# Optimization experiments

Hardware: AMD Instinct MI355X
Metric: run time of the kernel (lower is better)

Reference implementation:

```python
import jax, jax.numpy as jnp
import numpy as np

BS = 2048   # batch, iterated sequentially (memory carried step to step)
M = 256     # memory_size
E = 128     # expanded_memory_emb_size
HS = 512    # summarizer_hidden_size
HA = 512    # shared_AC_hidden_size
HP = 256    # processor_hidden_size


def make_pe(max_len, d):
    # standard sinusoidal positional encoding [max_len, d]
    pos = np.arange(max_len, dtype=np.float32)[:, None]
    div = np.exp(np.arange(0, d, 2, dtype=np.float32) * (-np.log(10000.0) / d))
    pe = np.zeros((max_len, d), dtype=np.float32)
    pe[:, 0::2] = np.sin(pos * div)
    pe[:, 1::2] = np.cos(pos * div)
    return jnp.asarray(pe)


def setup_inputs() -> dict:
    key = jax.random.key(0)
    ks = jax.random.split(key, 32)

    def n(k, sh, s=0.05):
        return jax.random.normal(k, sh, dtype=jnp.float32) * s

    return {
        "state": jax.random.normal(ks[0], (BS, 4), dtype=jnp.float32),
        "memory0": jax.random.uniform(ks[1], (M, E), dtype=jnp.float32),  # buffer init U(0,1)
        # embedder: Linear(4, E)
        "W_emb": n(ks[2], (4, E)), "b_emb": n(ks[3], (E,)),
        # reader Summarizer MLP: E -> HS -> 1
        "Wr1": n(ks[4], (E, HS)), "br1": n(ks[5], (HS,)),
        "Wr2": n(ks[6], (HS, 1)), "br2": n(ks[7], (1,)),
        # writer Summarizer MLP: E -> HS -> M
        "Ww1": n(ks[8], (E, HS)), "bw1": n(ks[9], (HS,)),
        "Ww2": n(ks[10], (HS, M)), "bw2": n(ks[11], (M,)),
        # shared AC trunk: 2E -> HA
        "Ws": n(ks[12], (2 * E, HA)), "bs_": n(ks[13], (HA,)),
        # actor: HA -> 5, critic: HA -> 1
        "Wa": n(ks[14], (HA, 5)), "ba": n(ks[15], (5,)),
        "Wc": n(ks[16], (HA, 1)), "bc": n(ks[17], (1,)),
        # processor: (5 + 1 + 2E) -> HP -> E
        "Wp1": n(ks[18], (5 + 1 + 2 * E, HP)), "bp1": n(ks[19], (HP,)),
        "Wp2": n(ks[20], (HP, E)), "bp2": n(ks[21], (E,)),
    }


def reference(state, memory0, W_emb, b_emb, Wr1, br1, Wr2, br2,
              Ww1, bw1, Ww2, bw2, Ws, bs_, Wa, ba, Wc, bc,
              Wp1, bp1, Wp2, bp2):
    pe_mem = make_pe(M, E)  # PE added to the M memory slots
    sg = jax.lax.stop_gradient

    def summarize(x, W1, b1, W2, b2):
        # Summarizer (MLP method): weight = softmax over token axis, z = weight^T x
        w = jax.nn.softmax(jax.nn.relu(x @ W1 + b1) @ W2 + b2, axis=0)  # [T, K]
        return w.T @ x  # [K, E]

    se = state @ W_emb + b_emb  # embed once: [BS, E]

    def step(mem, s):
        # reader over [current state ; PE(memory)] -> single summary token
        xr = jnp.concatenate([s[None, :], mem + pe_mem], axis=0)        # [M+1, E]
        mem_state = summarize(xr, Wr1, br1, Wr2, br2)[0]                # [E]
        cstate = jnp.concatenate([s, mem_state])                        # concat=True -> [2E]
        h = jax.nn.relu(cstate @ Ws + bs_)                              # [HA]
        probs = jax.nn.softmax(h @ Wa + ba)                             # [5]
        val = h @ Wc + bc                                               # [1]
        pin = jnp.concatenate([s, mem_state, probs, val])               # [2E+6]
        ms2 = jax.nn.relu(pin @ Wp1 + bp1) @ Wp2 + bp2                  # processed mem_state [E]
        # writer sees detached state / mem_state / memory (torch .detach())
        xw = jnp.concatenate([sg(s)[None, :], sg(ms2)[None, :], sg(mem) + pe_mem], axis=0)  # [M+2, E]
        nm = summarize(xw, Ww1, bw1, Ww2, bw2)                          # [M, E]
        nm = nm - nm.min(axis=-1, keepdims=True)
        nm = nm / nm.max(axis=-1, keepdims=True)
        return nm, (probs, val)

    _, (action_probs, state_values) = jax.lax.scan(step, memory0, se)
    return action_probs, state_values  # [BS, 5], [BS, 1]
```

## Files before the change

### kernel.cpp

```cpp
#include <hip/hip_runtime.h>
#include <math.h>

#define BSZ 2048
#define MM  256
#define EE  128
#define HSS 512
#define HPP 256
#define NOWN 64
#define NBLK 129
#define LEADER 128
#define TPB 512
#define ROWS 4

typedef float f4 __attribute__((ext_vector_type(4)));

#define OFF_PE   512
#define OFF_R0   (OFF_PE + MM*EE)
#define OFF_W0   (OFF_R0 + BSZ)
#define OFF_MP   (OFF_W0 + BSZ*MM)
#define OFF_SW   (OFF_MP + 2*MM*EE)
#define OFF_EV   (OFF_SW + 2*MM*MM)
#define OFF_ES   (OFF_EV + NOWN*EE)
#define OFF_MS2  (OFF_ES + NOWN)
#define OFF_CS   (OFF_MS2 + EE)
#define OFF_CBS  (OFF_CS + 4*HSS)
#define OFF_CP   (OFF_CBS + HSS)
#define OFF_CBP  (OFF_CP + 4*HPP)
#define OFF_BD   (OFF_CBP + HPP)
#define OFF_BP   (OFF_BD + NOWN*ROWS)

struct KParams {
  const float *state, *mem0, *Wemb, *bemb, *Wr1, *br1, *Wr2, *br2;
  const float *Ww1, *bw1, *Ww2, *bw2, *Ws, *bs, *Wa, *ba, *Wc, *bc;
  const float *Wp1, *bp1, *Wp2, *bp2;
  float *out;
  float *ws;
};

__device__ __forceinline__ float ldA(const float* p) {
  return __hip_atomic_load(p, __ATOMIC_RELAXED, __HIP_MEMORY_SCOPE_AGENT);
}
__device__ __forceinline__ void stA(float* p, float v) {
  __hip_atomic_store(p, v, __ATOMIC_RELAXED, __HIP_MEMORY_SCOPE_AGENT);
}
__device__ __forceinline__ unsigned ldAu(const unsigned* p) {
  return __hip_atomic_load(p, __ATOMIC_RELAXED, __HIP_MEMORY_SCOPE_AGENT);
}
__device__ __forceinline__ void stAu(unsigned* p, unsigned v) {
  __hip_atomic_store(p, v, __ATOMIC_RELAXED, __HIP_MEMORY_SCOPE_AGENT);
}

__device__ __forceinline__ void ldA4x8(const float* p, int strideF, f4* v) {
  const float *p1=p+strideF, *p2=p+2*strideF, *p3=p+3*strideF,
              *p4=p+4*strideF, *p5=p+5*strideF, *p6=p+6*strideF, *p7=p+7*strideF;
  asm volatile(
    "global_load_dwordx4 %0, %8, off sc0 sc1\n\t"
    "global_load_dwordx4 %1, %9, off sc0 sc1\n\t"
    "global_load_dwordx4 %2, %10, off sc0 sc1\n\t"
    "global_load_dwordx4 %3, %11, off sc0 sc1\n\t"
    "global_load_dwordx4 %4, %12, off sc0 sc1\n\t"
    "global_load_dwordx4 %5, %13, off sc0 sc1\n\t"
    "global_load_dwordx4 %6, %14, off sc0 sc1\n\t"
    "global_load_dwordx4 %7, %15, off sc0 sc1\n\t"
    "s_waitcnt vmcnt(0)"
    : "=&v"(v[0]), "=&v"(v[1]), "=&v"(v[2]), "=&v"(v[3]),
      "=&v"(v[4]), "=&v"(v[5]), "=&v"(v[6]), "=&v"(v[7])
    : "v"(p), "v"(p1), "v"(p2), "v"(p3), "v"(p4), "v"(p5), "v"(p6), "v"(p7)
    : "memory");
}
__device__ __forceinline__ void ldA4x4(const float* p, int strideF, f4* v) {
  const float *p1=p+strideF, *p2=p+2*strideF, *p3=p+3*strideF;
  asm volatile(
    "global_load_dwordx4 %0, %4, off sc0 sc1\n\t"
    "global_load_dwordx4 %1, %5, off sc0 sc1\n\t"
    "global_load_dwordx4 %2, %6, off sc0 sc1\n\t"
    "global_load_dwordx4 %3, %7, off sc0 sc1\n\t"
    "s_waitcnt vmcnt(0)"
    : "=&v"(v[0]), "=&v"(v[1]), "=&v"(v[2]), "=&v"(v[3])
    : "v"(p), "v"(p1), "v"(p2), "v"(p3)
    : "memory");
}
__device__ __forceinline__ f4 ldA4(const float* p) {
  f4 r;
  asm volatile("global_load_dwordx4 %0, %1, off sc0 sc1\n\ts_waitcnt vmcnt(0)"
    : "=&v"(r) : "v"(p) : "memory");
  return r;
}

__device__ __forceinline__ void drainSync() {
  asm volatile("s_waitcnt vmcnt(0)" ::: "memory");
  __syncthreads();
}

__device__ __forceinline__ float brs(float v, float* s8, int tid) {
  for (int o = 32; o > 0; o >>= 1) v += __shfl_down(v, o, 64);
  __syncthreads();
  if ((tid & 63) == 0) s8[tid >> 6] = v;
  __syncthreads();
  float r = s8[0]+s8[1]+s8[2]+s8[3]+s8[4]+s8[5]+s8[6]+s8[7];
  __syncthreads();
  return r;
}

template<int N>
__device__ __forceinline__ void brsN(float* v, float* sred, int tid) {
  #pragma unroll
  for (int k = 0; k < N; ++k)
    for (int o = 32; o > 0; o >>= 1) v[k] += __shfl_down(v[k], o, 64);
  __syncthreads();
  if ((tid & 63) == 0) {
    const int w = tid >> 6;
    #pragma unroll
    for (int k = 0; k < N; ++k) sred[k*8 + w] = v[k];
  }
  __syncthreads();
  #pragma unroll
  for (int k = 0; k < N; ++k) {
    float s = sred[k*8 + 0];
    #pragma unroll
    for (int w = 1; w < 8; ++w) s += sred[k*8 + w];
    v[k] = s;
  }
  __syncthreads();
}

__global__ __launch_bounds__(TPB)
void toyac_kernel(KParams p) {
  const int g = blockIdx.x;
  const int tid = threadIdx.x;
  float* ws = p.ws;
  unsigned* bar = (unsigned*)p.ws;
  const int og = (g >= NOWN && g < LEADER) ? (g - NOWN) : g;
  const int c0 = ROWS * ((g < NOWN) ? g : og);

  __shared__ float sX[ROWS][EE];
  __shared__ float sBuf[8192];
  __shared__ float sH4[ROWS][HSS];
  __shared__ float sHms[HSS];
  __shared__ float sEv[ROWS][MM];
  __shared__ float sRed[16];
  __shared__ float s8[8];
  __shared__ float sR48[48];
  __shared__ float sMS[EE];
  __shared__ float sMS2[EE];
  __shared__ float sSE[EE];
  __shared__ float sP1[HPP];
  __shared__ float sHv[HSS];
  __shared__ float sD[ROWS];
  __shared__ float sSm[32];

  const int hq = (tid & 127) * 4;
  const int eg4 = tid >> 7;

  if (g < NOWN) {
    const int e = tid & 127, r = tid >> 7, c = c0 + r;
    double dv = exp(-(double)(2*(e>>1)) * log(10000.0) / 128.0);
    double arg = (double)c * dv;
    float pev = ((e & 1) == 0) ? (float)sin(arg) : (float)cos(arg);
    ws[OFF_PE + (size_t)c*EE + e] = pev;
    float m0v = p.mem0[(size_t)c*EE + e] + pev;
    stA(ws + OFF_MP + (size_t)c*EE + e, m0v);
    sX[r][e] = m0v;
  } else if (g == LEADER) {
    for (int jj = tid; jj < HSS; jj += TPB) {
      float a0=0.f,a1=0.f,a2=0.f,a3=0.f,cb=0.f;
      for (int e = 0; e < EE; ++e) {
        float wv = p.Ws[(size_t)e*HSS + jj];
        a0 += p.Wemb[e]*wv; a1 += p.Wemb[EE+e]*wv;
        a2 += p.Wemb[2*EE+e]*wv; a3 += p.Wemb[3*EE+e]*wv;
        cb += p.bemb[e]*wv;
      }
      ws[OFF_CS + jj] = a0; ws[OFF_CS + HSS + jj] = a1;
      ws[OFF_CS + 2*HSS + jj] = a2; ws[OFF_CS + 3*HSS + jj] = a3;
      ws[OFF_CBS + jj] = cb;
    }
    if (tid < HPP) {
      int k = tid;
      float a0=0.f,a1=0.f,a2=0.f,a3=0.f,cb=0.f;
      for (int e = 0; e < EE; ++e) {
        float wv = p.Wp1[(size_t)e*HPP + k];
        a0 += p.Wemb[e]*wv; a1 += p.Wemb[EE+e]*wv;
        a2 += p.Wemb[2*EE+e]*wv; a3 += p.Wemb[3*EE+e]*wv;
        cb += p.bemb[e]*wv;
      }
      ws[OFF_CP + k] = a0; ws[OFF_CP + HPP + k] = a1;
      ws[OFF_CP + 2*HPP + k] = a2; ws[OFF_CP + 3*HPP + k] = a3;
      ws[OFF_CBP + k] = cb;
    }
  }

  for (int t = g; t < BSZ; t += NBLK) {
    __syncthreads();
    if (tid < EE) {
      const float* st = p.state + (size_t)t*4;
      sSE[tid] = st[0]*p.Wemb[tid] + st[1]*p.Wemb[EE+tid]
               + st[2]*p.Wemb[2*EE+tid] + st[3]*p.Wemb[3*EE+tid] + p.bemb[tid];
    }
    __syncthreads();
    {
      f4 a = {0.f,0.f,0.f,0.f};
      const float* base = p.Wr1 + (size_t)(eg4*32)*HSS + hq;
      for (int i = 0; i < 32; ++i)
        a += sSE[eg4*32 + i] * (*(const f4*)(base + (size_t)i*HSS));
      *(f4*)(sBuf + (size_t)eg4*HSS + hq) = a;
      __syncthreads();
      int h = tid;
      float hid = sBuf[h] + sBuf[HSS+h] + sBuf[2*HSS+h] + sBuf[3*HSS+h] + p.br1[h];
      float v = fmaxf(hid, 0.f) * p.Wr2[h];
      float sc = brs(v, s8, tid);
      if (tid == 0) stA(ws + OFF_R0 + t, sc + p.br2[0]);
      __syncthreads();
    }
    {
      f4 a = {0.f,0.f,0.f,0.f};
      const float* base = p.Ww1 + (size_t)(eg4*32)*HSS + hq;
      for (int i = 0; i < 32; ++i)
        a += sSE[eg4*32 + i] * (*(const f4*)(base + (size_t)i*HSS));
      *(f4*)(sBuf + (size_t)eg4*HSS + hq) = a;
      __syncthreads();
      int h = tid;
      sHv[h] = fmaxf(sBuf[h] + sBuf[HSS+h] + sBuf[2*HSS+h] + sBuf[3*HSS+h] + p.bw1[h], 0.f);
      __syncthreads();
      const int cq = (tid & 63) * 4, hg = tid >> 6;
      f4 q = {0.f,0.f,0.f,0.f};
      const float* b2 = p.Ww2 + (size_t)(hg*64)*MM + cq;
      for (int i = 0; i < 64; ++i)
        q += sHv[hg*64 + i] * (*(const f4*)(b2 + (size_t)i*MM));
      *(f4*)(sBuf + (size_t)hg*MM + cq) = q;
      __syncthreads();
      if (tid < MM) {
        float s = 0.f;
        #pragma unroll
        for (int k = 0; k < 8; ++k) s += sBuf[(size_t)k*MM + tid];
        stA(ws + OFF_W0 + (size_t)t*MM + tid, s + p.bw2[tid]);
      }
      __syncthreads();
    }
  }

  auto stageA = [&]() {
    {
      f4 a0={0.f,0.f,0.f,0.f},a1=a0,a2=a0,a3=a0;
      const float* base = p.Wr1 + (size_t)(eg4*32)*HSS + hq;
      for (int i = 0; i < 32; ++i) {
        f4 w = *(const f4*)(base + (size_t)i*HSS);
        int e = eg4*32 + i;
        a0 += sX[0][e]*w; a1 += sX[1][e]*w; a2 += sX[2][e]*w; a3 += sX[3][e]*w;
      }
      *(f4*)(sBuf + ((size_t)eg4*ROWS + 0)*HSS + hq) = a0;
      *(f4*)(sBuf + ((size_t)eg4*ROWS + 1)*HSS + hq) = a1;
      *(f4*)(sBuf + ((size_t)eg4*ROWS + 2)*HSS + hq) = a2;
      *(f4*)(sBuf + ((size_t)eg4*ROWS + 3)*HSS + hq) = a3;
    }
    __syncthreads();
    float es[ROWS];
    {
      int h = tid;
      float b = p.br1[h], wr = p.Wr2[h];
      float sc[ROWS];
      #pragma unroll
      for (int r = 0; r < ROWS; ++r) {
        float hid = sBuf[(0*ROWS+r)*HSS+h] + sBuf[(1*ROWS+r)*HSS+h]
                  + sBuf[(2*ROWS+r)*HSS+h] + sBuf[(3*ROWS+r)*HSS+h] + b;
        sc[r] = fmaxf(hid, 0.f) * wr;
      }
      brsN<ROWS>(sc, sR48, tid);
      #pragma unroll
      for (int r = 0; r < ROWS; ++r) es[r] = expf(sc[r] + p.br2[0]);
    }
    if (tid < EE) {
      float v = es[0]*sX[0][tid] + es[1]*sX[1][tid] + es[2]*sX[2][tid] + es[3]*sX[3][tid];
      stA(ws + OFF_EV + (size_t)g*EE + tid, v);
    }
    if (tid == 0) stA(ws + OFF_ES + g, es[0]+es[1]+es[2]+es[3]);
  };

  auto stageC = [&](float* swdst) {
    {
      f4 a0={0.f,0.f,0.f,0.f},a1=a0,a2=a0,a3=a0;
      const float* base = p.Ww1 + (size_t)(eg4*32)*HSS + hq;
      for (int i = 0; i < 32; ++i) {
        f4 w = *(const f4*)(base + (size_t)i*HSS);
        int e = eg4*32 + i;
        a0 += sX[0][e]*w; a1 += sX[1][e]*w; a2 += sX[2][e]*w; a3 += sX[3][e]*w;
      }
      *(f4*)(sBuf + ((size_t)eg4*ROWS + 0)*HSS + hq) = a0;
      *(f4*)(sBuf + ((size_t)eg4*ROWS + 1)*HSS + hq) = a1;
      *(f4*)(sBuf + ((size_t)eg4*ROWS + 2)*HSS + hq) = a2;
      *(f4*)(sBuf + ((size_t)eg4*ROWS + 3)*HSS + hq) = a3;
    }
    __syncthreads();
    {
      int h = tid;
      float b = p.bw1[h];
      #pragma unroll
      for (int r = 0; r < ROWS; ++r)
        sH4[r][h] = fmaxf(sBuf[(0*ROWS+r)*HSS+h] + sBuf[(1*ROWS+r)*HSS+h]
                        + sBuf[(2*ROWS+r)*HSS+h] + sBuf[(3*ROWS+r)*HSS+h] + b, 0.f);
    }
    __syncthreads();
    {
      const int cq = (tid & 63) * 4, hg = tid >> 6;
      f4 q0={0.f,0.f,0.f,0.f},q1=q0,q2=q0,q3=q0;
      const float* b2 = p.Ww2 + (size_t)(hg*64)*MM + cq;
      for (int i = 0; i < 64; ++i) {
        f4 w = *(const f4*)(b2 + (size_t)i*MM);
        int h = hg*64 + i;
        q0 += sH4[0][h]*w; q1 += sH4[1][h]*w; q2 += sH4[2][h]*w; q3 += sH4[3][h]*w;
      }
      *(f4*)(sBuf + ((size_t)hg*ROWS + 0)*MM + cq) = q0;
      *(f4*)(sBuf + ((size_t)hg*ROWS + 1)*MM + cq) = q1;
      *(f4*)(sBuf + ((size_t)hg*ROWS + 2)*MM + cq) = q2;
      *(f4*)(sBuf + ((size_t)hg*ROWS + 3)*MM + cq) = q3;
    }
    __syncthreads();
    {
      const int col = tid & 255, rp = tid >> 8;
      #pragma unroll
      for (int rr = 0; rr < 2; ++rr) {
        int r = rp*2 + rr;
        float s = 0.f;
        #pragma unroll
        for (int k = 0; k < 8; ++k) s += sBuf[((size_t)k*ROWS + r)*MM + col];
        stA(swdst + (size_t)(c0 + r)*MM + col, s + p.bw2[col]);
      }
    }
  };

  auto dBulkH = [&](int t) {
    float* swc = ws + OFF_SW + (size_t)(t&1)*MM*MM;
    float* mpc = ws + OFF_MP + (size_t)(t&1)*MM*EE;
    float ex[ROWS] = {0.f,0.f,0.f,0.f};
    if (tid < MM) {
      f4 s = ldA4(swc + (size_t)tid*MM + c0);
      #pragma unroll
      for (int r = 0; r < ROWS; ++r) { ex[r] = expf(s[r]); sEv[r][tid] = ex[r]; }
    }
    brsN<ROWS>(ex, sR48, tid);
    if (tid == 0) {
      stA(ws + OFF_BD + og*ROWS + 0, ex[0]);
      stA(ws + OFF_BD + og*ROWS + 1, ex[1]);
      stA(ws + OFF_BD + og*ROWS + 2, ex[2]);
      stA(ws + OFF_BD + og*ROWS + 3, ex[3]);
    }
    {
      const int e4 = (tid & 31) * 4, rg = tid >> 5;
      f4 a0={0.f,0.f,0.f,0.f},a1=a0,a2=a0,a3=a0;
      const float* base = mpc + (size_t)(rg*16)*EE + e4;
      f4 vv[8];
      ldA4x8(base, EE, vv);
      #pragma unroll
      for (int i = 0; i < 8; ++i) {
        int r0 = rg*16 + i;
        a0 += sEv[0][r0]*vv[i]; a1 += sEv[1][r0]*vv[i];
        a2 += sEv[2][r0]*vv[i]; a3 += sEv[3][r0]*vv[i];
      }
      ldA4x8(base + 8*EE, EE, vv);
      #pragma unroll
      for (int i = 0; i < 8; ++i) {
        int r0 = rg*16 + 8 + i;
        a0 += sEv[0][r0]*vv[i]; a1 += sEv[1][r0]*vv[i];
        a2 += sEv[2][r0]*vv[i]; a3 += sEv[3][r0]*vv[i];
      }
      *(f4*)(sBuf + ((size_t)0*16 + rg)*EE + e4) = a0;
      *(f4*)(sBuf + ((size_t)1*16 + rg)*EE + e4) = a1;
      *(f4*)(sBuf + ((size_t)2*16 + rg)*EE + e4) = a2;
      *(f4*)(sBuf + ((size_t)3*16 + rg)*EE + e4) = a3;
    }
    __syncthreads();
    {
      const int e = tid & 127, r = tid >> 7;
      float s = 0.f;
      #pragma unroll
      for (int q = 0; q < 16; ++q) s += sBuf[((size_t)r*16 + q)*EE + e];
      stA(ws + OFF_BP + ((size_t)og*ROWS + r)*EE + e, s);
    }
  };

  if (g == LEADER) {
    for (int t = 0; t < BSZ; ++t) {
      if (tid < NOWN) {
        while (ldAu(&bar[64+tid]) < (unsigned)(t+1)) __builtin_amdgcn_s_sleep(1);
      }
      __syncthreads();
      const float* st = p.state + (size_t)t*4;
      const float s0 = st[0], s1 = st[1], s2 = st[2], s3 = st[3];
      if (tid < EE)
        sSE[tid] = s0*p.Wemb[tid] + s1*p.Wemb[EE+tid]
                 + s2*p.Wemb[2*EE+tid] + s3*p.Wemb[3*EE+tid] + p.bemb[tid];
      float er0 = expf(ldA(ws + OFF_R0 + t));
      float v = (tid < NOWN) ? ldA(ws + OFF_ES + tid) : 0.f;
      float invd = 1.f / (er0 + brs(v, s8, tid));
      {
        const int e4 = (tid & 31) * 4, qg = tid >> 5;
        f4 vv[4];
        ldA4x4(ws + OFF_EV + (size_t)(qg*4)*EE + e4, EE, vv);
        f4 acc = vv[0]+vv[1]+vv[2]+vv[3];
        *(f4*)(sBuf + (size_t)qg*EE + e4) = acc;
      }
      __syncthreads();
      if (tid < EE) {
        float s = 0.f;
        #pragma unroll
        for (int q = 0; q < 16; ++q) s += sBuf[(size_t)q*EE + tid];
        sMS[tid] = (er0*sSE[tid] + s) * invd;
      }
      __syncthreads();
      {
        f4 a = {0.f,0.f,0.f,0.f};
        const float* base = p.Ws + (size_t)(EE + eg4*32)*HSS + hq;
        for (int i = 0; i < 32; ++i)
          a += sMS[eg4*32 + i] * (*(const f4*)(base + (size_t)i*HSS));
        *(f4*)(sBuf + (size_t)eg4*HSS + hq) = a;
      }
      __syncthreads();
      {
        int j = tid;
        const float* cs = ws + OFF_CS;
        float sh0 = s0*cs[j] + s1*cs[HSS+j] + s2*cs[2*HSS+j] + s3*cs[3*HSS+j] + ws[OFF_CBS + j];
        float hv = sBuf[j] + sBuf[HSS+j] + sBuf[2*HSS+j] + sBuf[3*HSS+j] + sh0 + p.bs[j];
        sHv[j] = fmaxf(hv, 0.f);
      }
      __syncthreads();
      {
        int j = tid;
        float hv = sHv[j];
        float pa[6];
        #pragma unroll
        for (int aa = 0; aa < 5; ++aa) pa[aa] = hv * p.Wa[(size_t)j*5 + aa];
        pa[5] = hv * p.Wc[j];
        brsN<6>(pa, sR48, tid);
        if (tid == 0) {
          float l0=pa[0]+p.ba[0], l1=pa[1]+p.ba[1], l2=pa[2]+p.ba[2];
          float l3=pa[3]+p.ba[3], l4=pa[4]+p.ba[4];
          float mx = fmaxf(fmaxf(fmaxf(l0,l1),fmaxf(l2,l3)), l4);
          float e0=expf(l0-mx),e1=expf(l1-mx),e2=expf(l2-mx),e3=expf(l3-mx),e4v=expf(l4-mx);
          float is = 1.f/(e0+e1+e2+e3+e4v);
          float p0=e0*is,p1=e1*is,p2=e2*is,p3=e3*is,p4=e4v*is;
          p.out[(size_t)t*5+0]=p0; p.out[(size_t)t*5+1]=p1; p.out[(size_t)t*5+2]=p2;
          p.out[(size_t)t*5+3]=p3; p.out[(size_t)t*5+4]=p4;
          float val = pa[5] + p.bc[0];
          p.out[(size_t)BSZ*5 + t] = val;
          sSm[1]=p0; sSm[2]=p1; sSm[3]=p2; sSm[4]=p3; sSm[5]=p4; sSm[6]=val;
        }
        __syncthreads();
      }
      {
        const int cq = (tid & 63) * 4, eg8 = tid >> 6;
        f4 a = {0.f,0.f,0.f,0.f};
        const float* base = p.Wp1 + (size_t)(EE + eg8*16)*HPP + cq;
        for (int i = 0; i < 16; ++i)
          a += sMS[eg8*16 + i] * (*(const f4*)(base + (size_t)i*HPP));
        *(f4*)(sBuf + (size_t)eg8*HPP + cq) = a;
      }
      __syncthreads();
      if (tid < HPP) {
        int k = tid;
        const float* cp = ws + OFF_CP;
        float acc = s0*cp[k] + s1*cp[HPP+k] + s2*cp[2*HPP+k] + s3*cp[3*HPP+k]
                  + ws[OFF_CBP + k] + p.bp1[k];
        #pragma unroll
        for (int q = 0; q < 8; ++q) acc += sBuf[(size_t)q*HPP + k];
        #pragma unroll
        for (int aa = 0; aa < 5; ++aa) acc += sSm[1+aa] * p.Wp1[(size_t)(2*EE+aa)*HPP + k];
        acc += sSm[6] * p.Wp1[(size_t)(2*EE+5)*HPP + k];
        sP1[k] = fmaxf(acc, 0.f);
      }
      __syncthreads();
      {
        const int cq = (tid & 31) * 4, kg = tid >> 5;
        f4 a = {0.f,0.f,0.f,0.f};
        const float* base = p.Wp2 + (size_t)(kg*16)*EE + cq;
        for (int i = 0; i < 16; ++i)
          a += sP1[kg*16 + i] * (*(const f4*)(base + (size_t)i*EE));
        *(f4*)(sBuf + (size_t)kg*EE + cq) = a;
      }
      __syncthreads();
      if (tid < EE) {
        float s = 0.f;
        #pragma unroll
        for (int q = 0; q < 16; ++q) s += sBuf[(size_t)q*EE + tid];
        stA(ws + OFF_MS2 + tid, s + p.bp2[tid]);
      }
      drainSync();
      if (tid == 0) stAu(&bar[320], (unsigned)(t+1));
    }
  } else if (g < NOWN) {
    const f4 wcol = *(const f4*)(p.Ww2 + (size_t)tid*MM + c0);
    drainSync();
    if (tid == 0) stAu(&bar[g], 1u);
    stageA();
    drainSync();
    if (tid == 0) stAu(&bar[64+g], 1u);

    for (int t = 0; t < BSZ-1; ++t) {
      if (tid < EE) {
        const float* st = p.state + (size_t)t*4;
        sSE[tid] = st[0]*p.Wemb[tid] + st[1]*p.Wemb[EE+tid]
                 + st[2]*p.Wemb[2*EE+tid] + st[3]*p.Wemb[3*EE+tid] + p.bemb[tid];
      }
      if (tid == 0) {
        f4 w0 = ldA4(ws + OFF_W0 + (size_t)t*MM + c0);
        #pragma unroll
        for (int r = 0; r < ROWS; ++r) sSm[8+r] = expf(w0[r]);
      }
      if (tid == 0) {
        while (ldAu(&bar[320]) < (unsigned)(t+1)) __builtin_amdgcn_s_sleep(1);
      }
      __syncthreads();
      if (tid < EE) sMS2[tid] = ldA(ws + OFF_MS2 + tid);
      __syncthreads();
      {
        f4 a = {0.f,0.f,0.f,0.f};
        const float* base = p.Ww1 + (size_t)(eg4*32)*HSS + hq;
        for (int i = 0; i < 32; ++i)
          a += sMS2[eg4*32 + i] * (*(const f4*)(base + (size_t)i*HSS));
        *(f4*)(sBuf + (size_t)eg4*HSS + hq) = a;
      }
      __syncthreads();
      sHms[tid] = fmaxf(sBuf[tid] + sBuf[HSS+tid] + sBuf[2*HSS+tid] + sBuf[3*HSS+tid]
                        + p.bw1[tid], 0.f);
      __syncthreads();
      float swv[ROWS];
      {
        float hm = sHms[tid];
        swv[0] = hm*wcol.x; swv[1] = hm*wcol.y; swv[2] = hm*wcol.z; swv[3] = hm*wcol.w;
        brsN<ROWS>(swv, sR48, tid);
      }
      if (tid == 0) {
        while (ldAu(&bar[192+g]) < (unsigned)(t+1)) __builtin_amdgcn_s_sleep(1);
      }
      __syncthreads();
      if (tid == 0) {
        f4 d = ldA4(ws + OFF_BD + g*ROWS);
        sD[0]=d.x; sD[1]=d.y; sD[2]=d.z; sD[3]=d.w;
      }
      __syncthreads();
      {
        const int e = tid & 127, r = tid >> 7;
        float bp = ldA(ws + OFF_BP + ((size_t)g*ROWS + r)*EE + e);
        float ew1 = expf(swv[r] + p.bw2[c0+r]);
        float ew0 = sSm[8+r];
        float inv = 1.f / (sD[r] + ew0 + ew1);
        float x = (bp + ew0*sSE[e] + ew1*sMS2[e]) * inv;
        float mn = x, mx = x;
        #pragma unroll
        for (int o = 1; o < 64; o <<= 1) {
          mn = fminf(mn, __shfl_xor(mn, o, 64));
          mx = fmaxf(mx, __shfl_xor(mx, o, 64));
        }
        if ((tid & 63) == 0) { sRed[(tid>>6)*2] = mn; sRed[(tid>>6)*2+1] = mx; }
        __syncthreads();
        mn = fminf(sRed[4*r], sRed[4*r+2]);
        mx = fmaxf(sRed[4*r+1], sRed[4*r+3]);
        float xr = (x - mn) / (mx - mn) + ws[OFF_PE + (size_t)(c0+r)*EE + e];
        float* mpn = ws + OFF_MP + (size_t)((t+1)&1)*MM*EE;
        stA(mpn + (size_t)(c0+r)*EE + e, xr);
        sX[r][e] = xr;
      }
      drainSync();
      if (tid == 0) stAu(&bar[g], (unsigned)(t+2));
      stageA();
      drainSync();
      if (tid == 0) stAu(&bar[64+g], (unsigned)(t+2));
    }
  } else {
    float* mpB[2] = { ws + OFF_MP, ws + OFF_MP + (size_t)MM*EE };
    for (int t = 0; t < BSZ-1; ++t) {
      if (tid == 0) {
        while (ldAu(&bar[og]) < (unsigned)(t+1)) __builtin_amdgcn_s_sleep(1);
      }
      __syncthreads();
      {
        const int e = tid & 127, r = tid >> 7;
        sX[r][e] = ldA(mpB[t&1] + (size_t)(c0+r)*EE + e);
      }
      __syncthreads();
      stageC(ws + OFF_SW + (size_t)(t&1)*MM*MM);
      drainSync();
      if (tid == 0) stAu(&bar[128+og], (unsigned)(t+1));
      if (tid < 64) {
        while (ldAu(&bar[128+tid]) < (unsigned)(t+1)) __builtin_amdgcn_s_sleep(1);
      } else if (tid < 128) {
        while (ldAu(&bar[tid-64]) < (unsigned)(t+1)) __builtin_amdgcn_s_sleep(1);
      }
      __syncthreads();
      dBulkH(t);
      drainSync();
      if (tid == 0) stAu(&bar[192+og], (unsigned)(t+1));
    }
  }
}

extern "C" void kernel_launch(void* const* d_in, const int* in_sizes, int n_in,
                              void* d_out, int out_size, void* d_ws, size_t ws_size,
                              hipStream_t stream) {
  hipMemsetAsync(d_ws, 0, 2048, stream);
  KParams kp;
  kp.state = (const float*)d_in[0];
  kp.mem0  = (const float*)d_in[1];
  kp.Wemb  = (const float*)d_in[2];
  kp.bemb  = (const float*)d_in[3];
  kp.Wr1   = (const float*)d_in[4];
  kp.br1   = (const float*)d_in[5];
  kp.Wr2   = (const float*)d_in[6];
  kp.br2   = (const float*)d_in[7];
  kp.Ww1   = (const float*)d_in[8];
  kp.bw1   = (const float*)d_in[9];
  kp.Ww2   = (const float*)d_in[10];
  kp.bw2   = (const float*)d_in[11];
  kp.Ws    = (const float*)d_in[12];
  kp.bs    = (const float*)d_in[13];
  kp.Wa    = (const float*)d_in[14];
  kp.ba    = (const float*)d_in[15];
  kp.Wc    = (const float*)d_in[16];
  kp.bc    = (const float*)d_in[17];
  kp.Wp1   = (const float*)d_in[18];
  kp.bp1   = (const float*)d_in[19];
  kp.Wp2   = (const float*)d_in[20];
  kp.bp2   = (const float*)d_in[21];
  kp.out   = (float*)d_out;
  kp.ws    = (float*)d_ws;
  toyac_kernel<<<dim3(NBLK), dim3(TPB), 0, stream>>>(kp);
}
```

Measured before the change: 54.94 ms.

## Exploit linearity of new memory rows to precompute first-layer projections

The new memory row is an affine combination of the bulk term P, the state embedding, ms2 and a constant, followed by min-max scaling plus PE. The first summarizer layers (Wr1/Ww1) of the next step can therefore be assembled from precomputed projections: P·W, PE·W, state-embedding·W, ms2·W and the column sums, combined with four per-row scalars. This moves the Wr1/Ww1 matvecs off the serial critical path by computing P·W early, overlapped with waiting, and splits the ms2 projection across the 64 owner blocks with an extra barrier. In exchange it adds workspace buffers, more cross-block synchronisation, and possible floating-point reassociation differences.

Measured after the change: 57.19 ms. +4.1%, slower.

```diff
diff --git a/kernel.cpp b/kernel.cpp
--- a/kernel.cpp
+++ b/kernel.cpp
@@ -28,6 +28,17 @@
 #define OFF_CBP  (OFF_CP + 4*HPP)
 #define OFF_BD   (OFF_CBP + HPP)
 #define OFF_BP   (OFF_BD + NOWN*ROWS)
+#define OFF_PWR  (OFF_BP + NOWN*ROWS*EE)
+#define OFF_PWW  (OFF_PWR + MM*HSS)
+#define OFF_CSR  (OFF_PWW + MM*HSS)
+#define OFF_CSW  (OFF_CSR + HSS)
+#define OFF_CR   (OFF_CSW + HSS)
+#define OFF_CBR  (OFF_CR + 4*HSS)
+#define OFF_CW2  (OFF_CBR + HSS)
+#define OFF_CBW  (OFF_CW2 + 4*HSS)
+#define OFF_MSR  (OFF_CBW + HSS)
+#define OFF_MSW  (OFF_MSR + 2*HSS)
+#define OFF_SCAL (OFF_MSW + 2*HSS)
 
 struct KParams {
   const float *state, *mem0, *Wemb, *bemb, *Wr1, *br1, *Wr2, *br2;
@@ -133,11 +144,14 @@
   const int og = (g >= NOWN && g < LEADER) ? (g - NOWN) : g;
   const int c0 = ROWS * ((g < NOWN) ? g : og);
 
+  __shared__ float sBuf[8192];
   __shared__ float sX[ROWS][EE];
-  __shared__ float sBuf[8192];
+  __shared__ float sP[ROWS][EE];
+  __shared__ float sPE[ROWS][EE];
+  __shared__ float sPW[ROWS][HSS];
   __shared__ float sH4[ROWS][HSS];
-  __shared__ float sHms[HSS];
-  __shared__ float sEv[ROWS][MM];
+  __shared__ float sMSR[HSS];
+  __shared__ float sMSWv[HSS];
   __shared__ float sRed[16];
   __shared__ float s8[8];
   __shared__ float sR48[48];
@@ -145,19 +159,44 @@
   __shared__ float sMS2[EE];
   __shared__ float sSE[EE];
   __shared__ float sP1[HPP];
-  __shared__ float sHv[HSS];
   __shared__ float sD[ROWS];
-  __shared__ float sSm[32];
+  __shared__ float sSm[40];
+
+  float (*sEv)[MM] = (float(*)[MM])sH4;
+  float* sHv = &sH4[2][0];
 
   const int hq = (tid & 127) * 4;
   const int eg4 = tid >> 7;
+
+  auto streamPW = [&](const float* W, float (*src)[EE]) {
+    {
+      f4 a0={0.f,0.f,0.f,0.f},a1=a0,a2=a0,a3=a0;
+      const float* base = W + (size_t)(eg4*32)*HSS + hq;
+      for (int i = 0; i < 32; ++i) {
+        f4 w = *(const f4*)(base + (size_t)i*HSS);
+        int e = eg4*32 + i;
+        a0 += src[0][e]*w; a1 += src[1][e]*w; a2 += src[2][e]*w; a3 += src[3][e]*w;
+      }
+      *(f4*)(sBuf + ((size_t)eg4*ROWS + 0)*HSS + hq) = a0;
+      *(f4*)(sBuf + ((size_t)eg4*ROWS + 1)*HSS + hq) = a1;
+      *(f4*)(sBuf + ((size_t)eg4*ROWS + 2)*HSS + hq) = a2;
+      *(f4*)(sBuf + ((size_t)eg4*ROWS + 3)*HSS + hq) = a3;
+    }
+    __syncthreads();
+    #pragma unroll
+    for (int r = 0; r < ROWS; ++r)
+      sPW[r][tid] = sBuf[(0*ROWS+r)*HSS+tid] + sBuf[(1*ROWS+r)*HSS+tid]
+                  + sBuf[(2*ROWS+r)*HSS+tid] + sBuf[(3*ROWS+r)*HSS+tid];
+    __syncthreads();
+  };
 
   if (g < NOWN) {
     const int e = tid & 127, r = tid >> 7, c = c0 + r;
     double dv = exp(-(double)(2*(e>>1)) * log(10000.0) / 128.0);
     double arg = (double)c * dv;
     float pev = ((e & 1) == 0) ? (float)sin(arg) : (float)cos(arg);
-    ws[OFF_PE + (size_t)c*EE + e] = pev;
+    stA(ws + OFF_PE + (size_t)c*EE + e, pev);
+    sPE[r][e] = pev;
     float m0v = p.mem0[(size_t)c*EE + e] + pev;
     stA(ws + OFF_MP + (size_t)c*EE + e, m0v);
     sX[r][e] = m0v;
@@ -187,6 +226,24 @@
       ws[OFF_CP + 2*HPP + k] = a2; ws[OFF_CP + 3*HPP + k] = a3;
       ws[OFF_CBP + k] = cb;
     }
+    {
+      int j = tid;
+      float r0=0.f,r1=0.f,r2=0.f,r3=0.f,rb=0.f,rc=0.f;
+      float w0=0.f,w1=0.f,w2=0.f,w3=0.f,wb=0.f,wc=0.f;
+      for (int e = 0; e < EE; ++e) {
+        float wr = p.Wr1[(size_t)e*HSS + j];
+        float ww = p.Ww1[(size_t)e*HSS + j];
+        float we0=p.Wemb[e], we1=p.Wemb[EE+e], we2=p.Wemb[2*EE+e], we3=p.Wemb[3*EE+e], wbe=p.bemb[e];
+        r0+=we0*wr; r1+=we1*wr; r2+=we2*wr; r3+=we3*wr; rb+=wbe*wr; rc+=wr;
+        w0+=we0*ww; w1+=we1*ww; w2+=we2*ww; w3+=we3*ww; wb+=wbe*ww; wc+=ww;
+      }
+      stA(ws+OFF_CR+j, r0); stA(ws+OFF_CR+HSS+j, r1);
+      stA(ws+OFF_CR+2*HSS+j, r2); stA(ws+OFF_CR+3*HSS+j, r3);
+      stA(ws+OFF_CBR+j, rb); stA(ws+OFF_CSR+j, rc);
+      stA(ws+OFF_CW2+j, w0); stA(ws+OFF_CW2+HSS+j, w1);
+      stA(ws+OFF_CW2+2*HSS+j, w2); stA(ws+OFF_CW2+3*HSS+j, w3);
+      stA(ws+OFF_CBW+j, wb); stA(ws+OFF_CSW+j, wc);
+    }
   }
 
   for (int t = g; t < BSZ; t += NBLK) {
@@ -238,7 +295,7 @@
     }
   }
 
-  auto stageA = [&]() {
+  auto stageA_full = [&]() {
     {
       f4 a0={0.f,0.f,0.f,0.f},a1=a0,a2=a0,a3=a0;
       const float* base = p.Wr1 + (size_t)(eg4*32)*HSS + hq;
@@ -275,7 +332,34 @@
     if (tid == 0) stA(ws + OFF_ES + g, es[0]+es[1]+es[2]+es[3]);
   };
 
-  auto stageC = [&](float* swdst) {
+  auto ww2pass = [&](float* swdst) {
+    const int cq = (tid & 63) * 4, hg = tid >> 6;
+    f4 q0={0.f,0.f,0.f,0.f},q1=q0,q2=q0,q3=q0;
+    const float* b2 = p.Ww2 + (size_t)(hg*64)*MM + cq;
+    for (int i = 0; i < 64; ++i) {
+      f4 w = *(const f4*)(b2 + (size_t)i*MM);
+      int h = hg*64 + i;
+      q0 += sH4[0][h]*w; q1 += sH4[1][h]*w; q2 += sH4[2][h]*w; q3 += sH4[3][h]*w;
+    }
+    *(f4*)(sBuf + ((size_t)hg*ROWS + 0)*MM + cq) = q0;
+    *(f4*)(sBuf + ((size_t)hg*ROWS + 1)*MM + cq) = q1;
+    *(f4*)(sBuf + ((size_t)hg*ROWS + 2)*MM + cq) = q2;
+    *(f4*)(sBuf + ((size_t)hg*ROWS + 3)*MM + cq) = q3;
+    __syncthreads();
+    {
+      const int col = tid & 255, rp = tid >> 8;
+      #pragma unroll
+      for (int rr = 0; rr < 2; ++rr) {
+        int r = rp*2 + rr;
+        float s = 0.f;
+        #pragma unroll
+        for (int k = 0; k < 8; ++k) s += sBuf[((size_t)k*ROWS + r)*MM + col];
+        stA(swdst + (size_t)(c0 + r)*MM + col, s + p.bw2[col]);
+      }
+    }
+  };
+
+  auto stageC_full = [&](float* swdst) {
     {
       f4 a0={0.f,0.f,0.f,0.f},a1=a0,a2=a0,a3=a0;
       const float* base = p.Ww1 + (size_t)(eg4*32)*HSS + hq;
@@ -299,37 +383,12 @@
                         + sBuf[(2*ROWS+r)*HSS+h] + sBuf[(3*ROWS+r)*HSS+h] + b, 0.f);
     }
     __syncthreads();
-    {
-      const int cq = (tid & 63) * 4, hg = tid >> 6;
-      f4 q0={0.f,0.f,0.f,0.f},q1=q0,q2=q0,q3=q0;
-      const float* b2 = p.Ww2 + (size_t)(hg*64)*MM + cq;
-      for (int i = 0; i < 64; ++i) {
-        f4 w = *(const f4*)(b2 + (size_t)i*MM);
-        int h = hg*64 + i;
-        q0 += sH4[0][h]*w; q1 += sH4[1][h]*w; q2 += sH4[2][h]*w; q3 += sH4[3][h]*w;
-      }
-      *(f4*)(sBuf + ((size_t)hg*ROWS + 0)*MM + cq) = q0;
-      *(f4*)(sBuf + ((size_t)hg*ROWS + 1)*MM + cq) = q1;
-      *(f4*)(sBuf + ((size_t)hg*ROWS + 2)*MM + cq) = q2;
-      *(f4*)(sBuf + ((size_t)hg*ROWS + 3)*MM + cq) = q3;
-    }
-    __syncthreads();
-    {
-      const int col = tid & 255, rp = tid >> 8;
-      #pragma unroll
-      for (int rr = 0; rr < 2; ++rr) {
-        int r = rp*2 + rr;
-        float s = 0.f;
-        #pragma unroll
-        for (int k = 0; k < 8; ++k) s += sBuf[((size_t)k*ROWS + r)*MM + col];
-        stA(swdst + (size_t)(c0 + r)*MM + col, s + p.bw2[col]);
-      }
-    }
+    ww2pass(swdst);
   };
 
-  auto dBulkH = [&](int t) {
-    float* swc = ws + OFF_SW + (size_t)(t&1)*MM*MM;
-    float* mpc = ws + OFF_MP + (size_t)(t&1)*MM*EE;
+  auto dBulkH = [&](int tt) {
+    float* swc = ws + OFF_SW + (size_t)(tt&1)*MM*MM;
+    float* mpc = ws + OFF_MP + (size_t)(tt&1)*MM*EE;
     float ex[ROWS] = {0.f,0.f,0.f,0.f};
     if (tid < MM) {
       f4 s = ldA4(swc + (size_t)tid*MM + c0);
@@ -373,8 +432,10 @@
       float s = 0.f;
       #pragma unroll
       for (int q = 0; q < 16; ++q) s += sBuf[((size_t)r*16 + q)*EE + e];
+      sP[r][e] = s;
       stA(ws + OFF_BP + ((size_t)og*ROWS + r)*EE + e, s);
     }
+    __syncthreads();
   };
 
   if (g == LEADER) {
@@ -414,17 +475,16 @@
         *(f4*)(sBuf + (size_t)eg4*HSS + hq) = a;
       }
       __syncthreads();
+      float hv;
       {
         int j = tid;
         const float* cs = ws + OFF_CS;
         float sh0 = s0*cs[j] + s1*cs[HSS+j] + s2*cs[2*HSS+j] + s3*cs[3*HSS+j] + ws[OFF_CBS + j];
-        float hv = sBuf[j] + sBuf[HSS+j] + sBuf[2*HSS+j] + sBuf[3*HSS+j] + sh0 + p.bs[j];
-        sHv[j] = fmaxf(hv, 0.f);
+        hv = fmaxf(sBuf[j] + sBuf[HSS+j] + sBuf[2*HSS+j] + sBuf[3*HSS+j] + sh0 + p.bs[j], 0.f);
       }
       __syncthreads();
       {
         int j = tid;
-        float hv = sHv[j];
         float pa[6];
         #pragma unroll
         for (int aa = 0; aa < 5; ++aa) pa[aa] = hv * p.Wa[(size_t)j*5 + aa];
@@ -489,21 +549,16 @@
     const f4 wcol = *(const f4*)(p.Ww2 + (size_t)tid*MM + c0);
     drainSync();
     if (tid == 0) stAu(&bar[g], 1u);
-    stageA();
+    streamPW(p.Wr1, sPE);
+    #pragma unroll
+    for (int r = 0; r < ROWS; ++r)
+      ws[OFF_PWR + (size_t)(c0+r)*HSS + tid] = sPW[r][tid];
+    __syncthreads();
+    stageA_full();
     drainSync();
     if (tid == 0) stAu(&bar[64+g], 1u);
 
     for (int t = 0; t < BSZ-1; ++t) {
-      if (tid < EE) {
-        const float* st = p.state + (size_t)t*4;
-        sSE[tid] = st[0]*p.Wemb[tid] + st[1]*p.Wemb[EE+tid]
-                 + st[2]*p.Wemb[2*EE+tid] + st[3]*p.Wemb[3*EE+tid] + p.bemb[tid];
-      }
-      if (tid == 0) {
-        f4 w0 = ldA4(ws + OFF_W0 + (size_t)t*MM + c0);
-        #pragma unroll
-        for (int r = 0; r < ROWS; ++r) sSm[8+r] = expf(w0[r]);
-      }
       if (tid == 0) {
         while (ldAu(&bar[320]) < (unsigned)(t+1)) __builtin_amdgcn_s_sleep(1);
       }
@@ -511,22 +566,22 @@
       if (tid < EE) sMS2[tid] = ldA(ws + OFF_MS2 + tid);
       __syncthreads();
       {
-        f4 a = {0.f,0.f,0.f,0.f};
-        const float* base = p.Ww1 + (size_t)(eg4*32)*HSS + hq;
-        for (int i = 0; i < 32; ++i)
-          a += sMS2[eg4*32 + i] * (*(const f4*)(base + (size_t)i*HSS));
-        *(f4*)(sBuf + (size_t)eg4*HSS + hq) = a;
-      }
-      __syncthreads();
-      sHms[tid] = fmaxf(sBuf[tid] + sBuf[HSS+tid] + sBuf[2*HSS+tid] + sBuf[3*HSS+tid]
-                        + p.bw1[tid], 0.f);
-      __syncthreads();
-      float swv[ROWS];
-      {
-        float hm = sHms[tid];
-        swv[0] = hm*wcol.x; swv[1] = hm*wcol.y; swv[2] = hm*wcol.z; swv[3] = hm*wcol.w;
-        brsN<ROWS>(swv, sR48, tid);
-      }
+        const int h8 = tid >> 6, ee = tid & 63;
+        const int h = 8*g + h8;
+        float m1 = sMS2[ee], m2 = sMS2[ee+64];
+        float pr = m1*p.Wr1[(size_t)ee*HSS+h] + m2*p.Wr1[(size_t)(ee+64)*HSS+h];
+        float pw = m1*p.Ww1[(size_t)ee*HSS+h] + m2*p.Ww1[(size_t)(ee+64)*HSS+h];
+        for (int o = 32; o > 0; o >>= 1) {
+          pr += __shfl_down(pr, o, 64);
+          pw += __shfl_down(pw, o, 64);
+        }
+        if (ee == 0) {
+          stA(ws + OFF_MSR + (size_t)(t&1)*HSS + h, pr);
+          stA(ws + OFF_MSW + (size_t)(t&1)*HSS + h, pw);
+        }
+      }
+      drainSync();
+      if (tid == 0) stAu(&bar[256+g], (unsigned)(t+1));
       if (tid == 0) {
         while (ldAu(&bar[192+g]) < (unsigned)(t+1)) __builtin_amdgcn_s_sleep(1);
       }
@@ -534,15 +589,37 @@
       if (tid == 0) {
         f4 d = ldA4(ws + OFF_BD + g*ROWS);
         sD[0]=d.x; sD[1]=d.y; sD[2]=d.z; sD[3]=d.w;
-      }
-      __syncthreads();
+        f4 w0 = ldA4(ws + OFF_W0 + (size_t)t*MM + c0);
+        sSm[8+0]=expf(w0.x); sSm[8+1]=expf(w0.y); sSm[8+2]=expf(w0.z); sSm[8+3]=expf(w0.w);
+      }
       {
         const int e = tid & 127, r = tid >> 7;
-        float bp = ldA(ws + OFF_BP + ((size_t)g*ROWS + r)*EE + e);
+        sP[r][e] = ldA(ws + OFF_BP + ((size_t)g*ROWS + r)*EE + e);
+      }
+      __syncthreads();
+      streamPW(p.Wr1, sP);
+      if (tid < NOWN) {
+        while (ldAu(&bar[256+tid]) < (unsigned)(t+1)) __builtin_amdgcn_s_sleep(1);
+      }
+      __syncthreads();
+      sMSR[tid]  = ldA(ws + OFF_MSR + (size_t)(t&1)*HSS + tid);
+      sMSWv[tid] = ldA(ws + OFF_MSW + (size_t)(t&1)*HSS + tid);
+      __syncthreads();
+      float swv[ROWS];
+      {
+        float hm = fmaxf(sMSWv[tid] + p.bw1[tid], 0.f);
+        swv[0]=hm*wcol.x; swv[1]=hm*wcol.y; swv[2]=hm*wcol.z; swv[3]=hm*wcol.w;
+        brsN<ROWS>(swv, sR48, tid);
+      }
+      const float* st = p.state + (size_t)t*4;
+      {
+        const int e = tid & 127, r = tid >> 7;
         float ew1 = expf(swv[r] + p.bw2[c0+r]);
         float ew0 = sSm[8+r];
         float inv = 1.f / (sD[r] + ew0 + ew1);
-        float x = (bp + ew0*sSE[e] + ew1*sMS2[e]) * inv;
+        float se = st[0]*p.Wemb[e] + st[1]*p.Wemb[EE+e]
+                 + st[2]*p.Wemb[2*EE+e] + st[3]*p.Wemb[3*EE+e] + p.bemb[e];
+        float x = (sP[r][e] + ew0*se + ew1*sMS2[e]) * inv;
         float mn = x, mx = x;
         #pragma unroll
         for (int o = 1; o < 64; o <<= 1) {
@@ -553,41 +630,131 @@
         __syncthreads();
         mn = fminf(sRed[4*r], sRed[4*r+2]);
         mx = fmaxf(sRed[4*r+1], sRed[4*r+3]);
-        float xr = (x - mn) / (mx - mn) + ws[OFF_PE + (size_t)(c0+r)*EE + e];
+        float k = 1.f / (mx - mn);
+        float xr = (x - mn) * k + sPE[r][e];
         float* mpn = ws + OFF_MP + (size_t)((t+1)&1)*MM*EE;
         stA(mpn + (size_t)(c0+r)*EE + e, xr);
         sX[r][e] = xr;
+        if (tid < 4) {
+          int rr = tid;
+          float ew1b = expf(swv[rr] + p.bw2[c0+rr]);
+          float invb = 1.f / (sD[rr] + sSm[8+rr] + ew1b);
+          float mnb = fminf(sRed[4*rr], sRed[4*rr+2]);
+          float mxb = fmaxf(sRed[4*rr+1], sRed[4*rr+3]);
+          float kb = 1.f / (mxb - mnb);
+          float a = kb * invb;
+          float b = a * sSm[8+rr];
+          float c = a * ew1b;
+          float d = -mnb * kb;
+          stA(ws + OFF_SCAL + (size_t)(c0+rr)*4 + 0, a);
+          stA(ws + OFF_SCAL + (size_t)(c0+rr)*4 + 1, b);
+          stA(ws + OFF_SCAL + (size_t)(c0+rr)*4 + 2, c);
+          stA(ws + OFF_SCAL + (size_t)(c0+rr)*4 + 3, d);
+          sSm[16+rr*4+0]=a; sSm[16+rr*4+1]=b; sSm[16+rr*4+2]=c; sSm[16+rr*4+3]=d;
+        }
       }
       drainSync();
       if (tid == 0) stAu(&bar[g], (unsigned)(t+2));
-      stageA();
+      {
+        const int j = tid;
+        float seW = st[0]*ldA(ws+OFF_CR+j) + st[1]*ldA(ws+OFF_CR+HSS+j)
+                  + st[2]*ldA(ws+OFF_CR+2*HSS+j) + st[3]*ldA(ws+OFF_CR+3*HSS+j)
+                  + ldA(ws+OFF_CBR+j);
+        float csv = ldA(ws+OFF_CSR+j);
+        float br = p.br1[j], wr = p.Wr2[j];
+        float sc[ROWS];
+        #pragma unroll
+        for (int r = 0; r < ROWS; ++r) {
+          float pre = sSm[16+r*4+0]*sPW[r][j] + sSm[16+r*4+1]*seW
+                    + sSm[16+r*4+2]*sMSR[j] + sSm[16+r*4+3]*csv
+                    + ws[OFF_PWR + (size_t)(c0+r)*HSS + j] + br;
+          sc[r] = fmaxf(pre, 0.f) * wr;
+        }
+        brsN<ROWS>(sc, sR48, tid);
+        float es[ROWS];
+        #pragma unroll
+        for (int r = 0; r < ROWS; ++r) es[r] = expf(sc[r] + p.br2[0]);
+        if (tid < EE) {
+          float v = es[0]*sX[0][tid] + es[1]*sX[1][tid] + es[2]*sX[2][tid] + es[3]*sX[3][tid];
+          stA(ws + OFF_EV + (size_t)g*EE + tid, v);
+        }
+        if (tid == 0) stA(ws + OFF_ES + g, es[0]+es[1]+es[2]+es[3]);
+      }
       drainSync();
       if (tid == 0) stAu(&bar[64+g], (unsigned)(t+2));
     }
   } else {
-    float* mpB[2] = { ws + OFF_MP, ws + OFF_MP + (size_t)MM*EE };
-    for (int t = 0; t < BSZ-1; ++t) {
+    if (tid == 0) {
+      while (ldAu(&bar[og]) < 1u) __builtin_amdgcn_s_sleep(1);
+    }
+    __syncthreads();
+    {
+      const int e = tid & 127, r = tid >> 7;
+      sPE[r][e] = ldA(ws + OFF_PE + (size_t)(c0+r)*EE + e);
+      sX[r][e]  = ldA(ws + OFF_MP + (size_t)(c0+r)*EE + e);
+    }
+    __syncthreads();
+    streamPW(p.Ww1, sPE);
+    #pragma unroll
+    for (int r = 0; r < ROWS; ++r)
+      ws[OFF_PWW + (size_t)(c0+r)*HSS + tid] = sPW[r][tid];
+    __syncthreads();
+    stageC_full(ws + OFF_SW);
+    drainSync();
+    if (tid == 0) stAu(&bar[128+og], 1u);
+    if (tid < 64) {
+      while (ldAu(&bar[128+tid]) < 1u) __builtin_amdgcn_s_sleep(1);
+    } else if (tid < 128) {
+      while (ldAu(&bar[tid-64]) < 1u) __builtin_amdgcn_s_sleep(1);
+    }
+    __syncthreads();
+    dBulkH(0);
+    drainSync();
+    if (tid == 0) stAu(&bar[192+og], 1u);
+    streamPW(p.Ww1, sP);
+
+    for (int t = 0; t < BSZ-2; ++t) {
+      if (tid < NOWN) {
+        while (ldAu(&bar[256+tid]) < (unsigned)(t+1)) __builtin_amdgcn_s_sleep(1);
+      }
+      __syncthreads();
+      sMSWv[tid] = ldA(ws + OFF_MSW + (size_t)(t&1)*HSS + tid);
       if (tid == 0) {
-        while (ldAu(&bar[og]) < (unsigned)(t+1)) __builtin_amdgcn_s_sleep(1);
-      }
-      __syncthreads();
-      {
-        const int e = tid & 127, r = tid >> 7;
-        sX[r][e] = ldA(mpB[t&1] + (size_t)(c0+r)*EE + e);
-      }
-      __syncthreads();
-      stageC(ws + OFF_SW + (size_t)(t&1)*MM*MM);
+        while (ldAu(&bar[og]) < (unsigned)(t+2)) __builtin_amdgcn_s_sleep(1);
+      }
+      __syncthreads();
+      if (tid < 16) sSm[16+tid] = ldA(ws + OFF_SCAL + (size_t)c0*4 + tid);
+      __syncthreads();
+      {
+        const int j = tid;
+        const float* st = p.state + (size_t)t*4;
+        float seW = st[0]*ldA(ws+OFF_CW2+j) + st[1]*ldA(ws+OFF_CW2+HSS+j)
+                  + st[2]*ldA(ws+OFF_CW2+2*HSS+j) + st[3]*ldA(ws+OFF_CW2+3*HSS+j)
+                  + ldA(ws+OFF_CBW+j);
+        float csv = ldA(ws+OFF_CSW+j);
+        float bw = p.bw1[j];
+        #pragma unroll
+        for (int r = 0; r < ROWS; ++r) {
+          float pre = sSm[16+r*4+0]*sPW[r][j] + sSm[16+r*4+1]*seW
+                    + sSm[16+r*4+2]*sMSWv[j] + sSm[16+r*4+3]*csv
+                    + ws[OFF_PWW + (size_t)(c0+r)*HSS + j] + bw;
+          sH4[r][j] = fmaxf(pre, 0.f);
+        }
+      }
+      __syncthreads();
+      ww2pass(ws + OFF_SW + (size_t)((t+1)&1)*MM*MM);
       drainSync();
-      if (tid == 0) stAu(&bar[128+og], (unsigned)(t+1));
+      if (tid == 0) stAu(&bar[128+og], (unsigned)(t+2));
       if (tid < 64) {
-        while (ldAu(&bar[128+tid]) < (unsigned)(t+1)) __builtin_amdgcn_s_sleep(1);
+        while (ldAu(&bar[128+tid]) < (unsigned)(t+2)) __builtin_amdgcn_s_sleep(1);
       } else if (tid < 128) {
-        while (ldAu(&bar[tid-64]) < (unsigned)(t+1)) __builtin_amdgcn_s_sleep(1);
-      }
-      __syncthreads();
-      dBulkH(t);
+        while (ldAu(&bar[tid-64]) < (unsigned)(t+2)) __builtin_amdgcn_s_sleep(1);
+      }
+      __syncthreads();
+      dBulkH(t+1);
       drainSync();
-      if (tid == 0) stAu(&bar[192+og], (unsigned)(t+1));
+      if (tid == 0) stAu(&bar[192+og], (unsigned)(t+2));
+      streamPW(p.Ww1, sP);
     }
   }
 }
```
